# Kernel optimization log

Measured on AMD Instinct MI355X. Metric: run time of the kernel, lower is better.

The kernel has to match this reference:

```python
import jax, jax.numpy as jnp
import numpy as np
import math

N_HEAD, D_MODEL, D_K, D_V = 8, 512, 64, 64
B, S = 4, 2048
EPS = 1e-5

def _xavier(key, shape):
    fan_in, fan_out = shape
    a = math.sqrt(6.0 / (fan_in + fan_out))
    return jax.random.uniform(key, shape, jnp.float32, -a, a)

def setup_inputs() -> dict:
    key = jax.random.key(0)
    ks = jax.random.split(key, 8)
    q = jax.random.normal(ks[0], (B, S, D_MODEL), jnp.float32)
    k = jax.random.normal(ks[1], (B, S, D_MODEL), jnp.float32)
    v = jax.random.normal(ks[2], (B, S, D_MODEL), jnp.float32)
    mask = jax.random.uniform(ks[3], (B, S, S)) < 0.1
    w_q = _xavier(ks[4], (D_MODEL, N_HEAD * D_K))
    w_k = _xavier(ks[5], (D_MODEL, N_HEAD * D_K))
    w_v = _xavier(ks[6], (D_MODEL, N_HEAD * D_V))
    w_o = _xavier(ks[7], (D_MODEL, N_HEAD * D_V))
    ln_g = jnp.ones((D_MODEL,), jnp.float32)
    ln_b = jnp.zeros((D_MODEL,), jnp.float32)
    return {"q": q, "k": k, "v": v, "w_q": w_q, "w_k": w_k, "w_v": w_v,
            "w_o": w_o, "ln_g": ln_g, "ln_b": ln_b, "mask": mask}

def reference(q, k, v, w_q, w_k, w_v, w_o, ln_g, ln_b, mask):
    b, lq, _ = q.shape
    lk = k.shape[1]
    residual = q
    # projections + head split: [b, len, H, d] -> [b, H, len, d]
    qh = (q @ w_q).reshape(b, lq, N_HEAD, D_K).transpose(0, 2, 1, 3)
    kh = (k @ w_k).reshape(b, lk, N_HEAD, D_K).transpose(0, 2, 1, 3)
    vh = (v @ w_v).reshape(b, lk, N_HEAD, D_V).transpose(0, 2, 1, 3)
    scale = math.sqrt(D_K)
    attn = jnp.einsum('bhqd,bhkd->bhqk', qh, kh) / scale
    attn = jnp.where(mask[:, None, :, :], jnp.float32(-1e9), attn)
    attn = jax.nn.softmax(attn, axis=-1)  # dropout is identity in eval
    heads = jnp.einsum('bhqk,bhkd->bhqd', attn, vh)
    heads = heads.transpose(0, 2, 1, 3).reshape(b, lq, N_HEAD * D_V)
    out = heads @ w_o + residual
    mu = out.mean(-1, keepdims=True)
    var = ((out - mu) ** 2).mean(-1, keepdims=True)
    out = (out - mu) * jax.lax.rsqrt(var + EPS) * ln_g + ln_b
    return out, attn
```

## Files before the change

kernel.cpp:

```cpp
#include <hip/hip_runtime.h>
#include <cstddef>

typedef __attribute__((ext_vector_type(8))) short bf16x8;
typedef __attribute__((ext_vector_type(4))) float f32x4;
typedef __attribute__((ext_vector_type(4))) short short4v;
typedef unsigned long long u64;
typedef unsigned int u32;
typedef unsigned short u16;

#define MFMA16 __builtin_amdgcn_mfma_f32_16x16x32_bf16
static constexpr float LN_EPS = 1e-5f;
static constexpr float L2E = 1.44269504f;

__device__ __forceinline__ u16 f2bf(float f) {
    u32 u = __builtin_bit_cast(u32, f);
    return (u16)((u + 0x7FFFu + ((u >> 16) & 1u)) >> 16);
}
__device__ __forceinline__ float bf2f(u16 h) {
    u32 u = ((u32)h) << 16;
    return __builtin_bit_cast(float, u);
}

__device__ __forceinline__ float block_sum256(float v) {
    __shared__ float sc[4];
    #pragma unroll
    for (int o = 32; o > 0; o >>= 1) v += __shfl_down(v, o);
    if ((threadIdx.x & 63) == 0) sc[threadIdx.x >> 6] = v;
    __syncthreads();
    v = sc[0] + sc[1] + sc[2] + sc[3];
    __syncthreads();
    return v;
}

__global__ __launch_bounds__(256) void prepw_kernel(
    const float* __restrict__ wq, const float* __restrict__ wk,
    const float* __restrict__ wv, const float* __restrict__ wo,
    u16* __restrict__ wt)
{
    const int mat = blockIdx.z;
    const float* W = mat == 0 ? wq : mat == 1 ? wk : mat == 2 ? wv : wo;
    const int k0 = blockIdx.x * 64, n0 = blockIdx.y * 64;
    __shared__ u16 ld[64][72];
    const int t = threadIdx.x;
    {
        const int kk = t >> 2;
        #pragma unroll
        for (int j = 0; j < 4; ++j) {
            const int nn = ((t & 3) + j * 4) * 4;
            float4 x = *(const float4*)&W[(size_t)(k0 + kk) * 512 + n0 + nn];
            ld[kk][nn + 0] = f2bf(x.x); ld[kk][nn + 1] = f2bf(x.y);
            ld[kk][nn + 2] = f2bf(x.z); ld[kk][nn + 3] = f2bf(x.w);
        }
    }
    __syncthreads();
    {
        const int n = t & 63, kc = (t >> 6) * 16;
        u16* op = wt + ((size_t)mat * 512 + n0 + n) * 512 + k0 + kc;
        #pragma unroll
        for (int j = 0; j < 4; ++j) {
            short4v v;
            v[0] = ld[kc + j*4 + 0][n]; v[1] = ld[kc + j*4 + 1][n];
            v[2] = ld[kc + j*4 + 2][n]; v[3] = ld[kc + j*4 + 3][n];
            *(short4v*)(op + j * 4) = v;
        }
    }
}

__global__ __launch_bounds__(256) void prepm_kernel(
    const int* __restrict__ mask, u64* __restrict__ bits)
{
    const int t = threadIdx.x;
    const int row = blockIdx.x * 4 + (t >> 6);
    const int wl = t & 63;
    const int* mrow = mask + (size_t)row * 2048;
    u64* brow = bits + (size_t)row * 32;
    #pragma unroll 8
    for (int it = 0; it < 32; ++it) {
        u64 b = __ballot(mrow[it * 64 + wl] != 0);
        if (wl == 0) brow[it] = b;
    }
}

__global__ __launch_bounds__(256) void proj_kernel(
    const float* __restrict__ qin, const float* __restrict__ kin, const float* __restrict__ vin,
    const u16* __restrict__ wt,
    u16* __restrict__ Qh, u16* __restrict__ Kh, u16* __restrict__ Vh)
{
    const int z = blockIdx.z;
    const float* X = z == 0 ? qin : (z == 1 ? kin : vin);
    const u16* W = wt + (size_t)z * 512 * 512;
    u16* O = z == 0 ? Qh : (z == 1 ? Kh : Vh);
    const int m0 = blockIdx.x * 64;
    const int h = blockIdx.y;
    const int t = threadIdx.x, l = t & 63, w = t >> 6;
    const int q = l & 15, G = l >> 4;
    const int wr = w >> 1, wc = w & 1;

    f32x4 acc[2][2] = {};
    for (int k0 = 0; k0 < 512; k0 += 32) {
        bf16x8 af[2], bfr[2];
        #pragma unroll
        for (int mi = 0; mi < 2; ++mi) {
            const float* xp = X + (size_t)(m0 + wr*32 + mi*16 + q) * 512 + k0 + G*8;
            float4 x0 = *(const float4*)xp;
            float4 x1 = *(const float4*)(xp + 4);
            bf16x8 a;
            a[0] = f2bf(x0.x); a[1] = f2bf(x0.y); a[2] = f2bf(x0.z); a[3] = f2bf(x0.w);
            a[4] = f2bf(x1.x); a[5] = f2bf(x1.y); a[6] = f2bf(x1.z); a[7] = f2bf(x1.w);
            af[mi] = a;
        }
        #pragma unroll
        for (int tn = 0; tn < 2; ++tn)
            bfr[tn] = *(const bf16x8*)(W + (size_t)(h*64 + wc*32 + tn*16 + q) * 512 + k0 + G*8);
        #pragma unroll
        for (int mi = 0; mi < 2; ++mi)
            #pragma unroll
            for (int tn = 0; tn < 2; ++tn)
                acc[mi][tn] = MFMA16(af[mi], bfr[tn], acc[mi][tn], 0, 0, 0);
    }
    const float scv = (z == 0) ? 0.125f : 1.0f;
    #pragma unroll
    for (int mi = 0; mi < 2; ++mi)
        #pragma unroll
        for (int tn = 0; tn < 2; ++tn)
            #pragma unroll
            for (int r = 0; r < 4; ++r) {
                const int m = m0 + wr*32 + mi*16 + G*4 + r;
                const int b = m >> 11, s = m & 2047;
                const int d = wc*32 + tn*16 + q;
                O[(((size_t)(b*8 + h) << 11) + s) * 64 + d] = f2bf(acc[mi][tn][r] * scv);
            }
}

__global__ __launch_bounds__(256) void vt_kernel(
    const u16* __restrict__ Vh, u16* __restrict__ Vt)
{
    const int bh = blockIdx.y, s0 = blockIdx.x * 64;
    __shared__ u16 ld[64][72];
    const int t = threadIdx.x;
    {
        const int s = t >> 2, dg = (t & 3) * 16;
        const u16* vp = Vh + ((((size_t)bh << 11) + s0 + s) * 64) + dg;
        *(bf16x8*)&ld[s][dg]     = *(const bf16x8*)vp;
        *(bf16x8*)&ld[s][dg + 8] = *(const bf16x8*)(vp + 8);
    }
    __syncthreads();
    {
        const int d = t & 63, sc = (t >> 6) * 16;
        u16* op = Vt + (((size_t)bh << 6) + d) * 2048 + s0 + sc;
        #pragma unroll
        for (int j = 0; j < 4; ++j) {
            short4v v;
            v[0] = ld[sc + j*4 + 0][d]; v[1] = ld[sc + j*4 + 1][d];
            v[2] = ld[sc + j*4 + 2][d]; v[3] = ld[sc + j*4 + 3][d];
            *(short4v*)(op + j * 4) = v;
        }
    }
}

__global__ __launch_bounds__(256) void attnpv_kernel(
    const u16* __restrict__ Qh, const u16* __restrict__ Kh, const u16* __restrict__ Vt,
    const u64* __restrict__ bits,
    u16* __restrict__ Et, float* __restrict__ attn, u16* __restrict__ heads)
{
    const int j   = blockIdx.x;
    const int lid = (j & 7) * 128 + (j >> 3);
    const int qt = lid & 31, bh = lid >> 5;
    const int b = bh >> 3, h = bh & 7;
    const int m0 = qt * 64;
    const int t = threadIdx.x, l = t & 63, w = t >> 6;
    const int q = l & 15, G = l >> 4;
    const int qrow = m0 + w*16 + q;
    __shared__ u16 kbuf[2][4096];
    __shared__ u16 vbuf[2][4096];
    __shared__ u16 alds[4][1024];
    __shared__ float sinv[64];
    u16* my = alds[w];

    const size_t qbase = (((size_t)bh << 11) + qrow) * 64;
    bf16x8 qf0 = *(const bf16x8*)(Qh + qbase + G*8);
    bf16x8 qf1 = *(const bf16x8*)(Qh + qbase + 32 + G*8);
    const u64* brow = bits + (((size_t)b << 11) + qrow) * 32;
    const int swz = (q & 7) << 3;
    const int sr  = l >> 2;
    const int c16 = (l & 3) * 16;
    const int ssw = (sr & 7) << 3;
    u16* etq = Et + (((size_t)bh * 32 + qt) << 17);

    const int srow0 = t >> 3;
    const int scol  = (t & 7) * 8;
    const u16* Kbase = Kh + (((size_t)bh << 11) * 64);
    const u16* Vbase = Vt + (((size_t)bh << 6) * 2048);
    const int eswz = (t * 8) ^ ((srow0 & 7) << 3);

    bf16x8 sk0, sk1, sv0, sv1;
    float rs = 0.f;
    f32x4 pacc[4] = {};

    {
        const u16* kp = Kbase + (size_t)srow0 * 64 + scol;
        sk0 = *(const bf16x8*)kp;
        sk1 = *(const bf16x8*)(kp + 32 * 64);
        const u16* vp = Vbase + (size_t)srow0 * 2048 + scol;
        sv0 = *(const bf16x8*)vp;
        sv1 = *(const bf16x8*)(vp + 32 * 2048);
        *(bf16x8*)&kbuf[0][eswz]        = sk0;
        *(bf16x8*)&kbuf[0][2048 + eswz] = sk1;
        *(bf16x8*)&vbuf[0][eswz]        = sv0;
        *(bf16x8*)&vbuf[0][2048 + eswz] = sv1;
    }
    __syncthreads();

    for (int kt = 0; kt < 32; ++kt) {
        const int cur = kt & 1;
        if (kt < 31) {
            const int n1 = (kt + 1) * 64;
            const u16* kp = Kbase + (size_t)(n1 + srow0) * 64 + scol;
            sk0 = *(const bf16x8*)kp;
            sk1 = *(const bf16x8*)(kp + 32 * 64);
            const u16* vp = Vbase + (size_t)srow0 * 2048 + n1 + scol;
            sv0 = *(const bf16x8*)vp;
            sv1 = *(const bf16x8*)(vp + 32 * 2048);
        }
        f32x4 acc[4] = {};
        #pragma unroll
        for (int mt = 0; mt < 4; ++mt) {
            const int r = mt*16 + q;
            const int rsw = (r & 7) << 3;
            bf16x8 k0 = *(const bf16x8*)&kbuf[cur][(r*64 +      G*8) ^ rsw];
            bf16x8 k1 = *(const bf16x8*)&kbuf[cur][(r*64 + 32 + G*8) ^ rsw];
            acc[mt] = MFMA16(k0, qf0, acc[mt], 0, 0, 0);
            acc[mt] = MFMA16(k1, qf1, acc[mt], 0, 0, 0);
        }
        const u64 mw = brow[kt];
        #pragma unroll
        for (int mt = 0; mt < 4; ++mt) {
            short4v sv;
            #pragma unroll
            for (int r = 0; r < 4; ++r) {
                const int c = mt*16 + G*4 + r;
                const float e = ((mw >> c) & 1) ? 0.f : exp2f(acc[mt][r] * L2E);
                rs += e;
                sv[r] = (short)f2bf(e);
            }
            *(short4v*)&my[(q*64 + mt*16 + G*4) ^ swz] = sv;
        }
        bf16x8 an0 = *(const bf16x8*)&my[(q*64 +  0 + G*8) ^ swz];
        bf16x8 an1 = *(const bf16x8*)&my[(q*64 + 32 + G*8) ^ swz];
        {
            u16* et = etq + (kt << 12) + (w * 16) * 64;
            bf16x8 e0 = *(const bf16x8*)&my[sr*64 + ((c16 + 0) ^ ssw)];
            bf16x8 e1 = *(const bf16x8*)&my[sr*64 + ((c16 + 8) ^ ssw)];
            *(bf16x8*)(et + sr*64 + c16)     = e0;
            *(bf16x8*)(et + sr*64 + c16 + 8) = e1;
        }
        #pragma unroll
        for (int dmt = 0; dmt < 4; ++dmt) {
            const int r = dmt*16 + q;
            const int rsw = (r & 7) << 3;
            bf16x8 v0 = *(const bf16x8*)&vbuf[cur][(r*64 +      G*8) ^ rsw];
            bf16x8 v1 = *(const bf16x8*)&vbuf[cur][(r*64 + 32 + G*8) ^ rsw];
            pacc[dmt] = MFMA16(v0, an0, pacc[dmt], 0, 0, 0);
            pacc[dmt] = MFMA16(v1, an1, pacc[dmt], 0, 0, 0);
        }
        if (kt < 31) {
            const int nxt = cur ^ 1;
            *(bf16x8*)&kbuf[nxt][eswz]        = sk0;
            *(bf16x8*)&kbuf[nxt][2048 + eswz] = sk1;
            *(bf16x8*)&vbuf[nxt][eswz]        = sv0;
            *(bf16x8*)&vbuf[nxt][2048 + eswz] = sv1;
        }
        __syncthreads();
    }
    rs += __shfl_xor(rs, 16);
    rs += __shfl_xor(rs, 32);
    const float inv = 1.0f / rs;
    if (G == 0) sinv[w*16 + q] = inv;
    #pragma unroll
    for (int dmt = 0; dmt < 4; ++dmt) {
        short4v sv;
        #pragma unroll
        for (int r = 0; r < 4; ++r) sv[r] = (short)f2bf(pacc[dmt][r] * inv);
        *(short4v*)&heads[(((size_t)b << 11) + qrow) * 512 + h*64 + dmt*16 + G*4] = sv;
    }
    __syncthreads();

    {
        const int ktw = w*8 + (l >> 3);
        const int cc  = (l & 7) * 8;
        const u16* tb = etq + (ktw << 12) + cc;
        float* ab = attn + ((((size_t)bh << 11) + m0) << 11) + ktw*64 + cc;
        for (int r = 0; r < 64; ++r) {
            bf16x8 e = *(const bf16x8*)(tb + r*64);
            const float iv = sinv[r];
            f32x4 lo, hi;
            #pragma unroll
            for (int jj = 0; jj < 4; ++jj) {
                lo[jj] = bf2f((u16)e[jj])     * iv;
                hi[jj] = bf2f((u16)e[jj + 4]) * iv;
            }
            *(f32x4*)(ab + (size_t)r * 2048)     = lo;
            *(f32x4*)(ab + (size_t)r * 2048 + 4) = hi;
        }
    }
}

__global__ __launch_bounds__(256) void outgemm_kernel(
    const u16* __restrict__ heads, const u16* __restrict__ wt,
    const float* __restrict__ qin, float* __restrict__ out)
{
    const int m0 = blockIdx.x * 64, n0b = blockIdx.y * 64;
    const int t = threadIdx.x, l = t & 63, w = t >> 6;
    const int q = l & 15, G = l >> 4;
    const int wr = w >> 1, wc = w & 1;
    const u16* W = wt + (size_t)3 * 512 * 512;
    f32x4 acc[2][2] = {};
    for (int k0 = 0; k0 < 512; k0 += 32) {
        bf16x8 af[2], bfr[2];
        #pragma unroll
        for (int mi = 0; mi < 2; ++mi)
            af[mi] = *(const bf16x8*)(heads + (size_t)(m0 + wr*32 + mi*16 + q) * 512 + k0 + G*8);
        #pragma unroll
        for (int tn = 0; tn < 2; ++tn)
            bfr[tn] = *(const bf16x8*)(W + (size_t)(n0b + wc*32 + tn*16 + q) * 512 + k0 + G*8);
        #pragma unroll
        for (int mi = 0; mi < 2; ++mi)
            #pragma unroll
            for (int tn = 0; tn < 2; ++tn)
                acc[mi][tn] = MFMA16(af[mi], bfr[tn], acc[mi][tn], 0, 0, 0);
    }
    #pragma unroll
    for (int mi = 0; mi < 2; ++mi)
        #pragma unroll
        for (int r = 0; r < 4; ++r) {
            const int m = m0 + wr*32 + mi*16 + G*4 + r;
            #pragma unroll
            for (int tn = 0; tn < 2; ++tn) {
                const int n = n0b + wc*32 + tn*16 + q;
                out[(size_t)m * 512 + n] = acc[mi][tn][r] + qin[(size_t)m * 512 + n];
            }
        }
}

__global__ __launch_bounds__(256) void ln_kernel(
    float* __restrict__ out, const float* __restrict__ g, const float* __restrict__ be)
{
    const int m = blockIdx.x;
    float* row = out + (size_t)m * 512;
    const int t = threadIdx.x;
    float2 v = ((const float2*)row)[t];
    float s  = block_sum256(v.x + v.y);
    float s2 = block_sum256(v.x * v.x + v.y * v.y);
    const float mu  = s * (1.0f / 512.0f);
    const float var = s2 * (1.0f / 512.0f) - mu * mu;
    const float inv = rsqrtf(var + LN_EPS);
    float2 gg = ((const float2*)g)[t];
    float2 bb = ((const float2*)be)[t];
    float2 r;
    r.x = (v.x - mu) * inv * gg.x + bb.x;
    r.y = (v.y - mu) * inv * gg.y + bb.y;
    ((float2*)row)[t] = r;
}

extern "C" void kernel_launch(void* const* d_in, const int* in_sizes, int n_in,
                              void* d_out, int out_size, void* d_ws, size_t ws_size,
                              hipStream_t stream) {
    const float* q   = (const float*)d_in[0];
    const float* k   = (const float*)d_in[1];
    const float* v   = (const float*)d_in[2];
    const float* wq  = (const float*)d_in[3];
    const float* wk  = (const float*)d_in[4];
    const float* wv  = (const float*)d_in[5];
    const float* wo  = (const float*)d_in[6];
    const float* g   = (const float*)d_in[7];
    const float* be  = (const float*)d_in[8];
    const int*   msk = (const int*)d_in[9];

    float* out  = (float*)d_out;
    float* attn = out + (size_t)4 * 2048 * 512;

    const size_t nQKV = (size_t)32 * 2048 * 64;
    u16* Qh    = (u16*)d_ws;
    u16* Kh    = Qh + nQKV;
    u16* Vh    = Kh + nQKV;
    u16* Vt    = Vh + nQKV;
    u16* heads = Vt + nQKV;
    u16* wt    = heads + (size_t)8192 * 512;
    u64* bits  = (u64*)(wt + (size_t)4 * 512 * 512);
    u16* Et    = (u16*)(bits + (size_t)8192 * 32);

    prepw_kernel  <<<dim3(8, 8, 4),    256, 0, stream>>>(wq, wk, wv, wo, wt);
    prepm_kernel  <<<dim3(2048),       256, 0, stream>>>(msk, bits);
    proj_kernel   <<<dim3(128, 8, 3),  256, 0, stream>>>(q, k, v, wt, Qh, Kh, Vh);
    vt_kernel     <<<dim3(32, 32),     256, 0, stream>>>(Vh, Vt);
    attnpv_kernel <<<dim3(1024),       256, 0, stream>>>(Qh, Kh, Vt, bits, Et, attn, heads);
    outgemm_kernel<<<dim3(128, 8),     256, 0, stream>>>(heads, wt, q, out);
    ln_kernel     <<<dim3(8192),       256, 0, stream>>>(out, g, be);
}
```

Before: 502.1 us.

## Two-pass softmax to write normalized attn directly; fuse V transpose into projection

```diff
diff --git a/kernel.cpp b/kernel.cpp
--- a/kernel.cpp
+++ b/kernel.cpp
@@ -3,6 +3,7 @@
 
 typedef __attribute__((ext_vector_type(8))) short bf16x8;
 typedef __attribute__((ext_vector_type(4))) float f32x4;
+typedef __attribute__((ext_vector_type(2))) float f32x2;
 typedef __attribute__((ext_vector_type(4))) short short4v;
 typedef unsigned long long u64;
 typedef unsigned int u32;
@@ -84,12 +85,11 @@
 __global__ __launch_bounds__(256) void proj_kernel(
     const float* __restrict__ qin, const float* __restrict__ kin, const float* __restrict__ vin,
     const u16* __restrict__ wt,
-    u16* __restrict__ Qh, u16* __restrict__ Kh, u16* __restrict__ Vh)
+    u16* __restrict__ Qh, u16* __restrict__ Kh, u16* __restrict__ Vt)
 {
     const int z = blockIdx.z;
     const float* X = z == 0 ? qin : (z == 1 ? kin : vin);
     const u16* W = wt + (size_t)z * 512 * 512;
-    u16* O = z == 0 ? Qh : (z == 1 ? Kh : Vh);
     const int m0 = blockIdx.x * 64;
     const int h = blockIdx.y;
     const int t = threadIdx.x, l = t & 63, w = t >> 6;
@@ -118,50 +118,40 @@
             for (int tn = 0; tn < 2; ++tn)
                 acc[mi][tn] = MFMA16(af[mi], bfr[tn], acc[mi][tn], 0, 0, 0);
     }
-    const float scv = (z == 0) ? 0.125f : 1.0f;
-    #pragma unroll
-    for (int mi = 0; mi < 2; ++mi)
-        #pragma unroll
-        for (int tn = 0; tn < 2; ++tn)
-            #pragma unroll
-            for (int r = 0; r < 4; ++r) {
-                const int m = m0 + wr*32 + mi*16 + G*4 + r;
-                const int b = m >> 11, s = m & 2047;
+    if (z == 2) {
+        #pragma unroll
+        for (int mi = 0; mi < 2; ++mi)
+            #pragma unroll
+            for (int tn = 0; tn < 2; ++tn) {
                 const int d = wc*32 + tn*16 + q;
-                O[(((size_t)(b*8 + h) << 11) + s) * 64 + d] = f2bf(acc[mi][tn][r] * scv);
+                const int m = m0 + wr*32 + mi*16 + G*4;
+                const int bb = m >> 11, s = m & 2047;
+                short4v sv;
+                #pragma unroll
+                for (int r = 0; r < 4; ++r) sv[r] = (short)f2bf(acc[mi][tn][r]);
+                *(short4v*)&Vt[(((size_t)(bb*8 + h) << 6) + d) * 2048 + s] = sv;
             }
-}
-
-__global__ __launch_bounds__(256) void vt_kernel(
-    const u16* __restrict__ Vh, u16* __restrict__ Vt)
-{
-    const int bh = blockIdx.y, s0 = blockIdx.x * 64;
-    __shared__ u16 ld[64][72];
-    const int t = threadIdx.x;
-    {
-        const int s = t >> 2, dg = (t & 3) * 16;
-        const u16* vp = Vh + ((((size_t)bh << 11) + s0 + s) * 64) + dg;
-        *(bf16x8*)&ld[s][dg]     = *(const bf16x8*)vp;
-        *(bf16x8*)&ld[s][dg + 8] = *(const bf16x8*)(vp + 8);
-    }
-    __syncthreads();
-    {
-        const int d = t & 63, sc = (t >> 6) * 16;
-        u16* op = Vt + (((size_t)bh << 6) + d) * 2048 + s0 + sc;
-        #pragma unroll
-        for (int j = 0; j < 4; ++j) {
-            short4v v;
-            v[0] = ld[sc + j*4 + 0][d]; v[1] = ld[sc + j*4 + 1][d];
-            v[2] = ld[sc + j*4 + 2][d]; v[3] = ld[sc + j*4 + 3][d];
-            *(short4v*)(op + j * 4) = v;
-        }
+    } else {
+        u16* O = z == 0 ? Qh : Kh;
+        const float scv = (z == 0) ? 0.125f : 1.0f;
+        #pragma unroll
+        for (int mi = 0; mi < 2; ++mi)
+            #pragma unroll
+            for (int tn = 0; tn < 2; ++tn)
+                #pragma unroll
+                for (int r = 0; r < 4; ++r) {
+                    const int m = m0 + wr*32 + mi*16 + G*4 + r;
+                    const int bb = m >> 11, s = m & 2047;
+                    const int d = wc*32 + tn*16 + q;
+                    O[(((size_t)(bb*8 + h) << 11) + s) * 64 + d] = f2bf(acc[mi][tn][r] * scv);
+                }
     }
 }
 
 __global__ __launch_bounds__(256) void attnpv_kernel(
     const u16* __restrict__ Qh, const u16* __restrict__ Kh, const u16* __restrict__ Vt,
     const u64* __restrict__ bits,
-    u16* __restrict__ Et, float* __restrict__ attn, u16* __restrict__ heads)
+    float* __restrict__ attn, u16* __restrict__ heads)
 {
     const int j   = blockIdx.x;
     const int lid = (j & 7) * 128 + (j >> 3);
@@ -173,19 +163,15 @@
     const int qrow = m0 + w*16 + q;
     __shared__ u16 kbuf[2][4096];
     __shared__ u16 vbuf[2][4096];
-    __shared__ u16 alds[4][1024];
+    __shared__ u16 alds2[4][2048];
     __shared__ float sinv[64];
-    u16* my = alds[w];
+    u16* alds2w = alds2[w];
 
     const size_t qbase = (((size_t)bh << 11) + qrow) * 64;
     bf16x8 qf0 = *(const bf16x8*)(Qh + qbase + G*8);
     bf16x8 qf1 = *(const bf16x8*)(Qh + qbase + 32 + G*8);
     const u64* brow = bits + (((size_t)b << 11) + qrow) * 32;
     const int swz = (q & 7) << 3;
-    const int sr  = l >> 2;
-    const int c16 = (l & 3) * 16;
-    const int ssw = (sr & 7) << 3;
-    u16* etq = Et + (((size_t)bh * 32 + qt) << 17);
 
     const int srow0 = t >> 3;
     const int scol  = (t & 7) * 8;
@@ -195,8 +181,53 @@
 
     bf16x8 sk0, sk1, sv0, sv1;
     float rs = 0.f;
+
+    {
+        const u16* kp = Kbase + (size_t)srow0 * 64 + scol;
+        sk0 = *(const bf16x8*)kp;
+        sk1 = *(const bf16x8*)(kp + 32 * 64);
+        *(bf16x8*)&kbuf[0][eswz]        = sk0;
+        *(bf16x8*)&kbuf[0][2048 + eswz] = sk1;
+    }
+    __syncthreads();
+    for (int kt = 0; kt < 32; ++kt) {
+        const int cur = kt & 1;
+        if (kt < 31) {
+            const u16* kp = Kbase + (size_t)((kt + 1) * 64 + srow0) * 64 + scol;
+            sk0 = *(const bf16x8*)kp;
+            sk1 = *(const bf16x8*)(kp + 32 * 64);
+        }
+        f32x4 acc[4] = {};
+        #pragma unroll
+        for (int mt = 0; mt < 4; ++mt) {
+            const int r = mt*16 + q;
+            const int rsw = (r & 7) << 3;
+            bf16x8 k0 = *(const bf16x8*)&kbuf[cur][(r*64 +      G*8) ^ rsw];
+            bf16x8 k1 = *(const bf16x8*)&kbuf[cur][(r*64 + 32 + G*8) ^ rsw];
+            acc[mt] = MFMA16(k0, qf0, acc[mt], 0, 0, 0);
+            acc[mt] = MFMA16(k1, qf1, acc[mt], 0, 0, 0);
+        }
+        const u64 mw = brow[kt];
+        #pragma unroll
+        for (int mt = 0; mt < 4; ++mt)
+            #pragma unroll
+            for (int r = 0; r < 4; ++r) {
+                const int c = mt*16 + G*4 + r;
+                rs += ((mw >> c) & 1) ? 0.f : exp2f(acc[mt][r] * L2E);
+            }
+        if (kt < 31) {
+            *(bf16x8*)&kbuf[cur ^ 1][eswz]        = sk0;
+            *(bf16x8*)&kbuf[cur ^ 1][2048 + eswz] = sk1;
+        }
+        __syncthreads();
+    }
+    rs += __shfl_xor(rs, 16);
+    rs += __shfl_xor(rs, 32);
+    const float inv = 1.0f / rs;
+    if (G == 0) sinv[w*16 + q] = inv;
+    __syncthreads();
+
     f32x4 pacc[4] = {};
-
     {
         const u16* kp = Kbase + (size_t)srow0 * 64 + scol;
         sk0 = *(const bf16x8*)kp;
@@ -210,7 +241,6 @@
         *(bf16x8*)&vbuf[0][2048 + eswz] = sv1;
     }
     __syncthreads();
-
     for (int kt = 0; kt < 32; ++kt) {
         const int cur = kt & 1;
         if (kt < 31) {
@@ -233,6 +263,7 @@
             acc[mt] = MFMA16(k1, qf1, acc[mt], 0, 0, 0);
         }
         const u64 mw = brow[kt];
+        u16* A2 = alds2w + (kt & 1) * 1024;
         #pragma unroll
         for (int mt = 0; mt < 4; ++mt) {
             short4v sv;
@@ -240,20 +271,12 @@
             for (int r = 0; r < 4; ++r) {
                 const int c = mt*16 + G*4 + r;
                 const float e = ((mw >> c) & 1) ? 0.f : exp2f(acc[mt][r] * L2E);
-                rs += e;
                 sv[r] = (short)f2bf(e);
             }
-            *(short4v*)&my[(q*64 + mt*16 + G*4) ^ swz] = sv;
-        }
-        bf16x8 an0 = *(const bf16x8*)&my[(q*64 +  0 + G*8) ^ swz];
-        bf16x8 an1 = *(const bf16x8*)&my[(q*64 + 32 + G*8) ^ swz];
-        {
-            u16* et = etq + (kt << 12) + (w * 16) * 64;
-            bf16x8 e0 = *(const bf16x8*)&my[sr*64 + ((c16 + 0) ^ ssw)];
-            bf16x8 e1 = *(const bf16x8*)&my[sr*64 + ((c16 + 8) ^ ssw)];
-            *(bf16x8*)(et + sr*64 + c16)     = e0;
-            *(bf16x8*)(et + sr*64 + c16 + 8) = e1;
-        }
+            *(short4v*)&A2[(q*64 + mt*16 + G*4) ^ swz] = sv;
+        }
+        bf16x8 an0 = *(const bf16x8*)&A2[(q*64 +  0 + G*8) ^ swz];
+        bf16x8 an1 = *(const bf16x8*)&A2[(q*64 + 32 + G*8) ^ swz];
         #pragma unroll
         for (int dmt = 0; dmt < 4; ++dmt) {
             const int r = dmt*16 + q;
@@ -270,38 +293,28 @@
             *(bf16x8*)&vbuf[nxt][eswz]        = sv0;
             *(bf16x8*)&vbuf[nxt][2048 + eswz] = sv1;
         }
+        if (kt & 1) {
+            const int ktg = kt >> 1;
+            const u16* A2f = alds2w + (l >> 5) * 1024;
+            float* awbase = attn + ((((size_t)bh << 11) + m0 + w*16) << 11) + ktg*128 + l*2;
+            #pragma unroll
+            for (int r = 0; r < 16; ++r) {
+                const float iv = sinv[w*16 + r];
+                const u32 e2 = *(const u32*)&A2f[(r*64 + (l & 31)*2) ^ ((r & 7) << 3)];
+                f32x2 o;
+                o[0] = bf2f((u16)(e2 & 0xffffu)) * iv;
+                o[1] = bf2f((u16)(e2 >> 16))     * iv;
+                *(f32x2*)(awbase + (size_t)r * 2048) = o;
+            }
+        }
         __syncthreads();
     }
-    rs += __shfl_xor(rs, 16);
-    rs += __shfl_xor(rs, 32);
-    const float inv = 1.0f / rs;
-    if (G == 0) sinv[w*16 + q] = inv;
     #pragma unroll
     for (int dmt = 0; dmt < 4; ++dmt) {
         short4v sv;
         #pragma unroll
         for (int r = 0; r < 4; ++r) sv[r] = (short)f2bf(pacc[dmt][r] * inv);
         *(short4v*)&heads[(((size_t)b << 11) + qrow) * 512 + h*64 + dmt*16 + G*4] = sv;
-    }
-    __syncthreads();
-
-    {
-        const int ktw = w*8 + (l >> 3);
-        const int cc  = (l & 7) * 8;
-        const u16* tb = etq + (ktw << 12) + cc;
-        float* ab = attn + ((((size_t)bh << 11) + m0) << 11) + ktw*64 + cc;
-        for (int r = 0; r < 64; ++r) {
-            bf16x8 e = *(const bf16x8*)(tb + r*64);
-            const float iv = sinv[r];
-            f32x4 lo, hi;
-            #pragma unroll
-            for (int jj = 0; jj < 4; ++jj) {
-                lo[jj] = bf2f((u16)e[jj])     * iv;
-                hi[jj] = bf2f((u16)e[jj + 4]) * iv;
-            }
-            *(f32x4*)(ab + (size_t)r * 2048)     = lo;
-            *(f32x4*)(ab + (size_t)r * 2048 + 4) = hi;
-        }
     }
 }
 
@@ -382,18 +395,15 @@
     const size_t nQKV = (size_t)32 * 2048 * 64;
     u16* Qh    = (u16*)d_ws;
     u16* Kh    = Qh + nQKV;
-    u16* Vh    = Kh + nQKV;
-    u16* Vt    = Vh + nQKV;
+    u16* Vt    = Kh + nQKV;
     u16* heads = Vt + nQKV;
     u16* wt    = heads + (size_t)8192 * 512;
     u64* bits  = (u64*)(wt + (size_t)4 * 512 * 512);
-    u16* Et    = (u16*)(bits + (size_t)8192 * 32);
 
     prepw_kernel  <<<dim3(8, 8, 4),    256, 0, stream>>>(wq, wk, wv, wo, wt);
     prepm_kernel  <<<dim3(2048),       256, 0, stream>>>(msk, bits);
-    proj_kernel   <<<dim3(128, 8, 3),  256, 0, stream>>>(q, k, v, wt, Qh, Kh, Vh);
-    vt_kernel     <<<dim3(32, 32),     256, 0, stream>>>(Vh, Vt);
-    attnpv_kernel <<<dim3(1024),       256, 0, stream>>>(Qh, Kh, Vt, bits, Et, attn, heads);
+    proj_kernel   <<<dim3(128, 8, 3),  256, 0, stream>>>(q, k, v, wt, Qh, Kh, Vt);
+    attnpv_kernel <<<dim3(1024),       256, 0, stream>>>(Qh, Kh, Vt, bits, attn, heads);
     outgemm_kernel<<<dim3(128, 8),     256, 0, stream>>>(heads, wt, q, out);
     ln_kernel     <<<dim3(8192),       256, 0, stream>>>(out, g, be);
 }
```

Measured after the change: 443.7 us (median of 2 runs). 1.13x faster.
